# Kernel optimization log

Hardware: AMD Instinct MI355X
Metric: run time of the kernel (lower is better)

Reference implementation:

```python
import jax, jax.numpy as jnp
import numpy as np

SQRT3 = float(np.sqrt(3.0))
TWO_PI = float(2.0 * np.pi)


def _safe_sqrt(x):
    return jnp.sqrt(jnp.clip(x, 1e-5))


def _matern(Q):
    # Matern 3/2 on the (already halved) quadratic form, matching torch matern()
    t = SQRT3 * _safe_sqrt(Q)
    return (1.0 + t) * jnp.exp(-t)


def _pairwise_kernel(x1, kp1, x2, kp2, scale):
    """Fused prob_product_quad + prob_product_constant + matern.

    x: [B,N,2] coords; kp: [B,N,3] = (e00, e11, e01) of SPD 2x2 E per point.
    Returns K [B,N,M].
    """
    a1, b1, c1 = kp1[..., 0], kp1[..., 1], kp1[..., 2]  # e00, e11, e01
    a2, b2, c2 = kp2[..., 0], kp2[..., 1], kp2[..., 2]
    det1 = a1 * b1 - c1 * c1  # det2x2(E1) [B,N]
    det2 = a2 * b2 - c2 * c2  # [B,M]
    s00 = a1[:, :, None] + a2[:, None, :]  # E1_00 + E2_00  [B,N,M]
    s11 = b1[:, :, None] + b2[:, None, :]
    s01 = c1[:, :, None] + c2[:, None, :]
    sdet = s00 * s11 - s01 * s01  # det(E1+E2)
    d = x1[:, :, None, :] - x2[:, None, :, :]  # [B,N,M,2]
    d0, d1 = d[..., 0], d[..., 1]
    Q = (s11 * d0 * d0 - 2.0 * s01 * d0 * d1 + s00 * d1 * d1) / sdet * 0.5
    C = 2.0 * (det1 ** 0.25)[:, :, None] * (det2 ** 0.25)[:, None, :] / _safe_sqrt(sdet)
    return _matern(Q) * C * scale


def _diag_kernel(kp, scale):
    # diagonal_prob_product: Q = 0, C = 2*sqrt(det E)/safe_sqrt(det(2E))
    a, b, c = kp[..., 0], kp[..., 1], kp[..., 2]
    det = a * b - c * c
    det2E = 4.0 * det  # det(2E) for 2x2
    C = 2.0 * jnp.sqrt(det) / _safe_sqrt(det2E)
    Q = jnp.zeros_like(C)
    return C * _matern(Q) * scale  # [B,N]


def setup_inputs() -> dict:
    key = jax.random.key(0)
    ks = jax.random.split(key, 8)
    B, N, M = 2, 1024, 16384

    def kparams(k, n):
        u = jax.random.uniform(k, (B, n, 3), dtype=jnp.float32)
        a = 0.5 + u[..., 0]
        b = 0.5 + u[..., 1]
        c = 0.2 * (u[..., 2] - 0.5)  # |c| small -> SPD
        return jnp.stack([a, b, c], axis=-1)

    coords_train = jax.random.uniform(ks[0], (B, N, 2), dtype=jnp.float32) * 512.0 / 64.0
    coords_test = jax.random.uniform(ks[1], (B, M, 2), dtype=jnp.float32) * 512.0 / 64.0
    kernel_params_train = kparams(ks[2], N)
    kernel_params_test = kparams(ks[3], M)
    y_train = jax.random.uniform(ks[4], (B, N, 1), dtype=jnp.float32) * 10.0
    var = 0.01 + 0.1 * jax.random.uniform(ks[5], (B, N), dtype=jnp.float32)
    mean = jnp.zeros((B, 1, 1), dtype=jnp.float32)
    scale_param = jnp.zeros((1,), dtype=jnp.float32)
    return {
        "coords_train": coords_train,
        "kernel_params_train": kernel_params_train,
        "coords_test": coords_test,
        "kernel_params_test": kernel_params_test,
        "y_train": y_train,
        "var": var,
        "mean": mean,
        "scale_param": scale_param,
    }


def reference(coords_train, kernel_params_train, coords_test, kernel_params_test,
              y_train, var, mean, scale_param):
    scale_prior = 1.0
    scale = scale_prior * jnp.exp(scale_param[0])  # CovarianceModule.get_scale
    B, N = coords_train.shape[0], coords_train.shape[1]

    # CovarianceModule / CrossCovarianceModule / DiagonalCovarianceModule
    K_nn = _pairwise_kernel(coords_train, kernel_params_train,
                            coords_train, kernel_params_train, scale)  # [B,N,N]
    K_nm = _pairwise_kernel(coords_train, kernel_params_train,
                            coords_test, kernel_params_test, scale)    # [B,N,M]
    K_mm_diag = _diag_kernel(kernel_params_test, scale)                 # [B,M]

    # GpSparseModule: A = K_nn + diag(var); chol; alpha = A^{-1}(y-mean); NLML
    eye = jnp.eye(N, dtype=K_nn.dtype)
    A = K_nn + var[..., None] * eye
    L = jnp.linalg.cholesky(A)
    y_centered = y_train - mean
    alpha = jax.scipy.linalg.cho_solve((L, True), y_centered)  # [B,N,1]
    data_fit = jnp.sum(y_centered * alpha, axis=1)             # [B,1]
    data_term = 0.5 * jnp.sum(data_fit, axis=1)                # [B]
    complexity_term = jnp.sum(jnp.log(jnp.diagonal(L, axis1=-2, axis2=-1)), axis=1)
    constant_term = 0.5 * N * np.log(TWO_PI)
    nlml = data_term + complexity_term + constant_term

    # GpDenseModule: predictive mean/variance at test points
    pred_mean = mean + jnp.einsum('bnm,bnk->bmk', K_nm, alpha)  # [B,M,1]
    v = jax.scipy.linalg.cho_solve((L, True), K_nm)             # [B,N,M]
    pred_var = (K_mm_diag - jnp.sum(K_nm * v, axis=1))[..., None]  # [B,M,1]
    return pred_mean, pred_var, nlml
```

## Files before the change

### kernel.cpp

```cpp
#include <hip/hip_runtime.h>
#include <math.h>

namespace {
constexpr int kB = 2;
constexpr int kN = 1024;
constexpr int kM = 16384;
constexpr float kSqrt3 = 1.7320508075688772f;

constexpr size_t A_BYTES = (size_t)kB * kN * kN * 4;
constexpr size_t DG_BYTES = (size_t)kB * 8 * 128 * 128 * 4;
constexpr size_t Z_BYTES = (size_t)kB * kN * 4;
constexpr size_t LH_BYTES = (size_t)kB * kN * kN * 2;
constexpr size_t DH_BYTES = (size_t)kB * 8 * 128 * 128 * 2;
constexpr size_t A_OFF = 0;
constexpr size_t DG_OFF = A_OFF + A_BYTES;
constexpr size_t Z_OFF = DG_OFF + DG_BYTES;
constexpr size_t LH_OFF = Z_OFF + Z_BYTES;
constexpr size_t LL_OFF = LH_OFF + LH_BYTES;
constexpr size_t DH_OFF = LL_OFF + LH_BYTES;
constexpr size_t DL_OFF = DH_OFF + DH_BYTES;
constexpr size_t WS_BYTES = DL_OFF + DH_BYTES;
}

typedef __attribute__((ext_vector_type(8))) short short8v;
typedef __attribute__((ext_vector_type(4))) float floatx4;

__device__ __forceinline__ float b16f(unsigned short h) {
  return __uint_as_float(((unsigned)h) << 16);
}
__device__ __forceinline__ unsigned short b16rn(float x) {
  unsigned u = __float_as_uint(x);
  unsigned r = u + 0x7FFFu + ((u >> 16) & 1u);
  return (unsigned short)(r >> 16);
}
__device__ __forceinline__ void split_bf16(float x, unsigned short& h, unsigned short& l) {
  unsigned u = __float_as_uint(x);
  h = (unsigned short)(u >> 16);
  float rem = x - b16f(h);
  l = (unsigned short)(__float_as_uint(rem) >> 16);
}
__device__ __forceinline__ void pack2(float v0, float v1, unsigned& hw, unsigned& lw) {
  unsigned u0 = __float_as_uint(v0), u1 = __float_as_uint(v1);
  unsigned h0 = u0 & 0xFFFF0000u;
  unsigned h1 = u1 & 0xFFFF0000u;
  hw = (h0 >> 16) | h1;
  float r0 = v0 - __uint_as_float(h0);
  float r1 = v1 - __uint_as_float(h1);
  lw = (__float_as_uint(r0) >> 16) | (__float_as_uint(r1) & 0xFFFF0000u);
}

__device__ __forceinline__ float pair_kernel(
    float x0, float x1, float a1, float b1, float c1,
    float y0, float y1, float a2, float b2, float c2, float scale) {
  float det1 = a1 * b1 - c1 * c1;
  float det2 = a2 * b2 - c2 * c2;
  float s00 = a1 + a2, s11 = b1 + b2, s01 = c1 + c2;
  float sdet = s00 * s11 - s01 * s01;
  float d0 = x0 - y0, d1 = x1 - y1;
  float quad = s11 * d0 * d0 - 2.0f * s01 * d0 * d1 + s00 * d1 * d1;
  float Q = __fdividef(0.5f * quad, sdet);
  float x3 = 3.0f * fmaxf(Q, 1e-5f);
  float t = x3 * rsqrtf(x3);
  float C = 2.0f * sqrtf(sqrtf(det1)) * sqrtf(sqrtf(det2)) * rsqrtf(fmaxf(sdet, 1e-5f));
  return (1.0f + t) * __expf(-t) * C * scale;
}

__global__ __launch_bounds__(256) void build_A(
    const float* __restrict__ xt, const float* __restrict__ pt,
    const float* __restrict__ var, const float* __restrict__ sp,
    float* __restrict__ A) {
  int idx = blockIdx.x * 256 + threadIdx.x;
  int b = idx / (kN * kN);
  int r = (idx / kN) % kN;
  int c = idx % kN;
  float scale = __expf(sp[0]);
  const float* x1 = xt + ((size_t)b * kN + r) * 2;
  const float* p1 = pt + ((size_t)b * kN + r) * 3;
  const float* x2 = xt + ((size_t)b * kN + c) * 2;
  const float* p2 = pt + ((size_t)b * kN + c) * 3;
  float k = pair_kernel(x1[0], x1[1], p1[0], p1[1], p1[2],
                        x2[0], x2[1], p2[0], p2[1], p2[2], scale);
  if (r == c) k += var[b * kN + r];
  A[(size_t)idx] = k;
}

__device__ __forceinline__ void tri_decode(int idx, int& ti, int& tj) {
  float f = sqrtf(8.0f * (float)idx + 1.0f);
  int t0 = (int)((f - 1.0f) * 0.5f);
  while (t0 * (t0 + 1) / 2 > idx) --t0;
  while ((t0 + 1) * (t0 + 2) / 2 <= idx) ++t0;
  ti = t0;
  tj = idx - t0 * (t0 + 1) / 2;
}

__global__ __launch_bounds__(1024, 1) void chol_panel(float* __restrict__ A,
                                                      float* __restrict__ Dg,
                                                      unsigned short* __restrict__ Dh,
                                                      unsigned short* __restrict__ Dl, int p) {
  __shared__ float At[128 * 132];
  __shared__ float Dt[128 * 132];
  __shared__ float Tt[3 * 32 * 33];
  int b = blockIdx.x, t = threadIdx.x;
  float* Ab = A + (size_t)b * kN * kN;
  int r0 = p * 128;
#pragma unroll
  for (int q = 0; q < 4; ++q) {
    int idx = t + 1024 * q;
    int r = idx >> 5, c4 = idx & 31;
    *(float4*)&At[r * 132 + c4 * 4] = *(const float4*)&Ab[(size_t)(r0 + r) * kN + r0 + c4 * 4];
  }
  __syncthreads();
  int wave = t >> 6, lane = t & 63;
  int row0 = lane, row1 = lane + 64;
  for (int kb = 0; kb < 16; ++kb) {
    int K0 = kb * 8;
    int Kp = K0 - 8;
    if (kb > 0) {
      if (wave == 0) {
        int rr = lane >> 3, cc = lane & 7;
        float s = 0.0f;
#pragma unroll
        for (int e = 0; e < 8; ++e)
          s += At[(K0 + rr) * 132 + Kp + e] * At[(K0 + cc) * 132 + Kp + e];
        At[(K0 + rr) * 132 + K0 + cc] -= s;
      } else {
        int n = 120 - 8 * kb;
        int nt = n >> 2;
        int ntt = nt * (nt + 1) / 2;
        int base = K0 + 8;
        for (int idx = t - 64; idx < ntt; idx += 960) {
          int ti, tj;
          tri_decode(idx, ti, tj);
          int i0 = base + ti * 4, j0 = base + tj * 4;
          float Li[4][8], Lj[4][8];
#pragma unroll
          for (int r = 0; r < 4; ++r) {
            *(float4*)&Li[r][0] = *(const float4*)&At[(i0 + r) * 132 + Kp];
            *(float4*)&Li[r][4] = *(const float4*)&At[(i0 + r) * 132 + Kp + 4];
            *(float4*)&Lj[r][0] = *(const float4*)&At[(j0 + r) * 132 + Kp];
            *(float4*)&Lj[r][4] = *(const float4*)&At[(j0 + r) * 132 + Kp + 4];
          }
#pragma unroll
          for (int r = 0; r < 4; ++r) {
            float4 cv = *(const float4*)&At[(i0 + r) * 132 + j0];
            float cc4[4] = {cv.x, cv.y, cv.z, cv.w};
#pragma unroll
            for (int c = 0; c < 4; ++c) {
              float s = 0.0f;
#pragma unroll
              for (int e = 0; e < 8; ++e) s += Li[r][e] * Lj[c][e];
              cc4[c] -= s;
            }
            float4 ov = {cc4[0], cc4[1], cc4[2], cc4[3]};
            *(float4*)&At[(i0 + r) * 132 + j0] = ov;
          }
        }
      }
    }
    __syncthreads();
    if (wave == 0) {
      float rA0[8], rA1[8];
      *(float4*)&rA0[0] = *(const float4*)&At[row0 * 132 + K0];
      *(float4*)&rA0[4] = *(const float4*)&At[row0 * 132 + K0 + 4];
      *(float4*)&rA1[0] = *(const float4*)&At[row1 * 132 + K0];
      *(float4*)&rA1[4] = *(const float4*)&At[row1 * 132 + K0 + 4];
      if (kb > 0) {
        float pA0[8], pA1[8];
        *(float4*)&pA0[0] = *(const float4*)&At[row0 * 132 + Kp];
        *(float4*)&pA0[4] = *(const float4*)&At[row0 * 132 + Kp + 4];
        *(float4*)&pA1[0] = *(const float4*)&At[row1 * 132 + Kp];
        *(float4*)&pA1[4] = *(const float4*)&At[row1 * 132 + Kp + 4];
#pragma unroll
        for (int j = 0; j < 8; ++j) {
          float s0 = 0.0f, s1 = 0.0f;
#pragma unroll
          for (int e = 0; e < 8; ++e) {
            float pj = At[(K0 + j) * 132 + Kp + e];
            s0 += pA0[e] * pj;
            s1 += pA1[e] * pj;
          }
          rA0[j] -= s0;
          rA1[j] -= s1;
        }
      }
      float L11[8][8], idg[8];
#pragma unroll
      for (int r = 0; r < 8; ++r) {
        *(float4*)&L11[r][0] = *(const float4*)&At[(K0 + r) * 132 + K0];
        *(float4*)&L11[r][4] = *(const float4*)&At[(K0 + r) * 132 + K0 + 4];
      }
#pragma unroll
      for (int c = 0; c < 8; ++c) {
        float d = sqrtf(L11[c][c]);
        float iv = 1.0f / d;
        idg[c] = iv;
        L11[c][c] = d;
#pragma unroll
        for (int i = c + 1; i < 8; ++i) L11[i][c] *= iv;
#pragma unroll
        for (int j = c + 1; j < 8; ++j)
#pragma unroll
          for (int i = j; i < 8; ++i) L11[i][j] -= L11[i][c] * L11[j][c];
      }
      if (row0 >= K0 + 8) {
#pragma unroll
        for (int c = 0; c < 8; ++c) {
          float s = rA0[c];
#pragma unroll
          for (int j = 0; j < c; ++j) s -= rA0[j] * L11[c][j];
          rA0[c] = s * idg[c];
        }
      } else if (row0 >= K0) {
#pragma unroll
        for (int rr = 0; rr < 8; ++rr)
          if (row0 - K0 == rr) {
#pragma unroll
            for (int e = 0; e < 8; ++e) rA0[e] = (e <= rr) ? L11[rr][e] : 0.0f;
          }
      }
      if (row1 >= K0 + 8) {
#pragma unroll
        for (int c = 0; c < 8; ++c) {
          float s = rA1[c];
#pragma unroll
          for (int j = 0; j < c; ++j) s -= rA1[j] * L11[c][j];
          rA1[c] = s * idg[c];
        }
      } else if (row1 >= K0) {
#pragma unroll
        for (int rr = 0; rr < 8; ++rr)
          if (row1 - K0 == rr) {
#pragma unroll
            for (int e = 0; e < 8; ++e) rA1[e] = (e <= rr) ? L11[rr][e] : 0.0f;
          }
      }
      if (row0 >= K0) {
        float4 v0 = {rA0[0], rA0[1], rA0[2], rA0[3]};
        float4 v1 = {rA0[4], rA0[5], rA0[6], rA0[7]};
        *(float4*)&At[row0 * 132 + K0] = v0;
        *(float4*)&At[row0 * 132 + K0 + 4] = v1;
      }
      if (row1 >= K0) {
        float4 v0 = {rA1[0], rA1[1], rA1[2], rA1[3]};
        float4 v1 = {rA1[4], rA1[5], rA1[6], rA1[7]};
        *(float4*)&At[row1 * 132 + K0] = v0;
        *(float4*)&At[row1 * 132 + K0 + 4] = v1;
      }
    }
    __syncthreads();
  }
  if (t < 128) {
    int q = t >> 5, c = t & 31, bse = q * 32;
    float x[32];
#pragma unroll
    for (int r = 0; r < 32; ++r) {
      float s = (r == c) ? 1.0f : 0.0f;
#pragma unroll
      for (int j = 0; j < 32; ++j)
        if (j < r) s -= At[(bse + r) * 132 + bse + j] * x[j];
      x[r] = (r < c) ? 0.0f : s / At[(bse + r) * 132 + bse + r];
    }
#pragma unroll
    for (int r = 0; r < 32; ++r) Dt[(bse + r) * 132 + bse + c] = x[r];
  }
  __syncthreads();
  {
    int r = t >> 5, cl = t & 31;
    for (int s = 1; s <= 3; ++s) {
      for (int blk = 0; blk < 4 - s; ++blk) {
        int J = blk, I = J + s;
        float sum = 0.0f;
        for (int K = J; K < I; ++K)
          for (int j = 0; j < 32; ++j)
            sum += At[(I * 32 + r) * 132 + K * 32 + j] * Dt[(K * 32 + j) * 132 + J * 32 + cl];
        Tt[blk * (32 * 33) + r * 33 + cl] = sum;
      }
      __syncthreads();
      for (int blk = 0; blk < 4 - s; ++blk) {
        int J = blk, I = J + s;
        float sum = 0.0f;
        for (int j = 0; j < 32; ++j)
          sum += Dt[(I * 32 + r) * 132 + I * 32 + j] * Tt[blk * (32 * 33) + j * 33 + cl];
        Dt[(I * 32 + r) * 132 + J * 32 + cl] = -sum;
      }
      __syncthreads();
    }
  }
#pragma unroll
  for (int q = 0; q < 4; ++q) {
    int jj = t + 1024 * q;
    int r = jj >> 5, ch = jj & 31;
    int c0 = ch * 4;
    float4 v = *(const float4*)&At[r * 132 + c0];
    v.x = (c0 + 0 <= r) ? v.x : 0.0f;
    v.y = (c0 + 1 <= r) ? v.y : 0.0f;
    v.z = (c0 + 2 <= r) ? v.z : 0.0f;
    v.w = (c0 + 3 <= r) ? v.w : 0.0f;
    *(float4*)&Ab[(size_t)(r0 + r) * kN + r0 + c0] = v;
  }
  float* Db = Dg + (size_t)(b * 8 + p) * 16384;
  unsigned short* Dhb = Dh + (size_t)(b * 8 + p) * 16384;
  unsigned short* Dlb = Dl + (size_t)(b * 8 + p) * 16384;
#pragma unroll
  for (int q = 0; q < 4; ++q) {
    int jj = t + 1024 * q;
    int r = jj >> 5, ch = jj & 31;
    int c0 = ch * 4;
    float4 v = *(const float4*)&Dt[r * 132 + c0];
    v.x = (c0 + 0 <= r) ? v.x : 0.0f;
    v.y = (c0 + 1 <= r) ? v.y : 0.0f;
    v.z = (c0 + 2 <= r) ? v.z : 0.0f;
    v.w = (c0 + 3 <= r) ? v.w : 0.0f;
    *(float4*)&Db[r * 128 + c0] = v;
    float vv[4] = {v.x, v.y, v.z, v.w};
    unsigned short hs[4], ls[4];
#pragma unroll
    for (int e = 0; e < 4; ++e) split_bf16(vv[e], hs[e], ls[e]);
    *(ushort4*)&Dhb[r * 128 + c0] = make_ushort4(hs[0], hs[1], hs[2], hs[3]);
    *(ushort4*)&Dlb[r * 128 + c0] = make_ushort4(ls[0], ls[1], ls[2], ls[3]);
  }
}

__global__ __launch_bounds__(256) void chol_trsm(float* __restrict__ A,
                                                 const float* __restrict__ Dg,
                                                 unsigned short* __restrict__ Lh, int p) {
  __shared__ float At[128 * 129];
  __shared__ float Dt[128 * 129];
  int b = blockIdx.y, rb = blockIdx.x;
  int rs = (p + 1 + rb) * 128;
  float* Ab = A + (size_t)b * kN * kN;
  const float* Db = Dg + (size_t)(b * 8 + p) * 16384;
  int t = threadIdx.x;
  for (int q = 0; q < 64; ++q) {
    int li = t + 256 * q;
    int r = li >> 7, cc = li & 127;
    At[r * 129 + cc] = Ab[(size_t)(rs + r) * kN + p * 128 + cc];
    Dt[r * 129 + cc] = Db[r * 128 + cc];
  }
  __syncthreads();
  int tx = t & 15, ty = t >> 4;
  float acc[8][8] = {};
  for (int j = 0; j < 128; ++j) {
    float a[8], d[8];
#pragma unroll
    for (int q = 0; q < 8; ++q) a[q] = At[(ty * 8 + q) * 129 + j];
#pragma unroll
    for (int q = 0; q < 8; ++q) d[q] = Dt[(tx * 8 + q) * 129 + j];
#pragma unroll
    for (int qr = 0; qr < 8; ++qr)
#pragma unroll
      for (int qc = 0; qc < 8; ++qc) acc[qr][qc] = fmaf(a[qr], d[qc], acc[qr][qc]);
  }
#pragma unroll
  for (int qr = 0; qr < 8; ++qr)
#pragma unroll
    for (int qc = 0; qc < 8; ++qc) {
      float v = acc[qr][qc];
      Ab[(size_t)(rs + ty * 8 + qr) * kN + p * 128 + tx * 8 + qc] = v;
      size_t lo = ((size_t)b * kN + rs + ty * 8 + qr) * kN + p * 128 + tx * 8 + qc;
      Lh[lo] = b16rn(-v);
    }
}

__global__ __launch_bounds__(256) void chol_syrk(float* __restrict__ A, int p) {
  __shared__ float L1t[128 * 129];
  __shared__ float L2t[128 * 129];
  int b = blockIdx.y;
  int pid = blockIdx.x;
  int bi = 0;
  while ((bi + 1) * (bi + 2) / 2 <= pid) ++bi;
  int bj = pid - bi * (bi + 1) / 2;
  int rs1 = (p + 1 + bi) * 128, rs2 = (p + 1 + bj) * 128;
  float* Ab = A + (size_t)b * kN * kN;
  int t = threadIdx.x;
  for (int q = 0; q < 64; ++q) {
    int li = t + 256 * q;
    int r = li >> 7, cc = li & 127;
    L1t[r * 129 + cc] = Ab[(size_t)(rs1 + r) * kN + p * 128 + cc];
    L2t[r * 129 + cc] = Ab[(size_t)(rs2 + r) * kN + p * 128 + cc];
  }
  __syncthreads();
  int tx = t & 15, ty = t >> 4;
  float acc[8][8] = {};
  for (int j = 0; j < 128; ++j) {
    float a[8], d[8];
#pragma unroll
    for (int q = 0; q < 8; ++q) a[q] = L1t[(ty * 8 + q) * 129 + j];
#pragma unroll
    for (int q = 0; q < 8; ++q) d[q] = L2t[(tx * 8 + q) * 129 + j];
#pragma unroll
    for (int qr = 0; qr < 8; ++qr)
#pragma unroll
      for (int qc = 0; qc < 8; ++qc) acc[qr][qc] = fmaf(a[qr], d[qc], acc[qr][qc]);
  }
#pragma unroll
  for (int qr = 0; qr < 8; ++qr)
#pragma unroll
    for (int qc = 0; qc < 8; ++qc) {
      size_t o = (size_t)(rs1 + ty * 8 + qr) * kN + rs2 + tx * 8 + qc;
      Ab[o] -= acc[qr][qc];
    }
}

__global__ __launch_bounds__(1024) void solve_small(
    const float* __restrict__ A, const float* __restrict__ Dg,
    const float* __restrict__ y, const float* __restrict__ meanp,
    float* __restrict__ zbuf, float* __restrict__ out) {
  __shared__ float Ls[128 * 132];
  __shared__ __align__(16) float zs[1024];
  __shared__ float ts[128];
  __shared__ float part[128 * 9];
  __shared__ float red[1024];
  int b = blockIdx.x, t = threadIdx.x;
  int row = t & 127, g = t >> 7;
  const float* Ab = A + (size_t)b * kN * kN;
  float mv = meanp[b];
  zs[t] = y[b * kN + t] - mv;
  __syncthreads();
  for (int i = 0; i < 8; ++i) {
    float ps = 0.0f;
    for (int k = 0; k < i; ++k) {
#pragma unroll
      for (int q = 0; q < 4; ++q) {
        int li = t + 1024 * q;
        int r = li >> 5, c4 = li & 31;
        *(float4*)&Ls[r * 132 + c4 * 4] =
            *(const float4*)&Ab[(size_t)(i * 128 + r) * kN + k * 128 + c4 * 4];
      }
      __syncthreads();
      const float* Lr = &Ls[row * 132 + g * 16];
      const float* zk = &zs[k * 128 + g * 16];
#pragma unroll
      for (int c = 0; c < 16; c += 4) {
        float4 lv = *(const float4*)&Lr[c];
        float4 zv = *(const float4*)&zk[c];
        ps += lv.x * zv.x + lv.y * zv.y + lv.z * zv.z + lv.w * zv.w;
      }
      __syncthreads();
    }
    part[row * 9 + g] = ps;
    {
      const float* Db = Dg + (size_t)(b * 8 + i) * 16384;
#pragma unroll
      for (int q = 0; q < 4; ++q) {
        int li = t + 1024 * q;
        int r = li >> 5, c4 = li & 31;
        *(float4*)&Ls[r * 132 + c4 * 4] = *(const float4*)&Db[r * 128 + c4 * 4];
      }
    }
    __syncthreads();
    if (g == 0) {
      float acc = zs[i * 128 + row];
#pragma unroll
      for (int gg = 0; gg < 8; ++gg) acc -= part[row * 9 + gg];
      ts[row] = acc;
    }
    __syncthreads();
    float s = 0.0f;
    int c0 = g * 16, c1 = min(c0 + 16, row + 1);
    for (int c = c0; c < c1; ++c) s += Ls[row * 132 + c] * ts[c];
    part[row * 9 + g] = s;
    __syncthreads();
    if (g == 0) {
      float zv = 0.0f;
#pragma unroll
      for (int gg = 0; gg < 8; ++gg) zv += part[row * 9 + gg];
      zs[i * 128 + row] = zv;
    }
    __syncthreads();
  }
  red[t] = zs[t] * zs[t];
  __syncthreads();
  for (int s = 512; s > 0; s >>= 1) {
    if (t < s) red[t] += red[t + s];
    __syncthreads();
  }
  float dfs = red[0];
  __syncthreads();
  red[t] = logf(Ab[(size_t)t * kN + t]);
  __syncthreads();
  for (int s = 512; s > 0; s >>= 1) {
    if (t < s) red[t] += red[t + s];
    __syncthreads();
  }
  if (t == 0)
    out[2 * kB * kM + b] = 0.5f * dfs + red[0] + 0.5f * 1024.0f * logf(6.283185307179586f);
  zbuf[b * kN + t] = zs[t];
}

__global__ __launch_bounds__(256, 2) void fused_mfma(
    const unsigned short* __restrict__ Lh,
    const unsigned short* __restrict__ Dh, const unsigned short* __restrict__ Dl,
    const float* __restrict__ xt, const float* __restrict__ pt,
    const float* __restrict__ xs, const float* __restrict__ ps,
    const float* __restrict__ sp, const float* __restrict__ meanp,
    const float* __restrict__ zbuf, float* __restrict__ out) {
  __shared__ unsigned short Th[32 * 144];
  __shared__ unsigned short Tl[32 * 144];
  __shared__ float trp[128 * 6];
  __shared__ float tp[32 * 6];
  __shared__ float zs[128];
  __shared__ float red[32 * 16 * 2];
  int bid = blockIdx.x;
  int xcd = bid & 7;
  int b = xcd >> 2;
  int mt = (xcd & 3) * 128 + (bid >> 3);
  int t = threadIdx.x;
  int lane = t & 63, wave = t >> 6;
  int lrow = lane & 15, kgrp = lane >> 4;
  float scale = __expf(sp[0]);
  if (t < 32) {
    int mg = mt * 32 + t;
    float x0 = xs[((size_t)b * kM + mg) * 2 + 0];
    float x1 = xs[((size_t)b * kM + mg) * 2 + 1];
    float a = ps[((size_t)b * kM + mg) * 3 + 0];
    float bb = ps[((size_t)b * kM + mg) * 3 + 1];
    float c = ps[((size_t)b * kM + mg) * 3 + 2];
    float det2 = a * bb - c * c;
    tp[t * 6 + 0] = x0; tp[t * 6 + 1] = x1; tp[t * 6 + 2] = a;
    tp[t * 6 + 3] = bb; tp[t * 6 + 4] = c; tp[t * 6 + 5] = sqrtf(sqrtf(det2));
  }
  floatx4 W[8][2][2];
#pragma unroll
  for (int i = 0; i < 8; ++i)
#pragma unroll
    for (int rf = 0; rf < 2; ++rf)
#pragma unroll
      for (int cf = 0; cf < 2; ++cf) W[i][rf][cf] = (floatx4){0.f, 0.f, 0.f, 0.f};
  float pma[2] = {0.f, 0.f}, s2a[2] = {0.f, 0.f};

#define FUSED_K_STEP(KC)                                                                   \
  {                                                                                        \
    constexpr int k = (KC);                                                                \
    __syncthreads();                                                                       \
    if (t < 128) {                                                                         \
      size_t n = (size_t)b * kN + k * 128 + t;                                             \
      float x0 = xt[n * 2 + 0];                                                            \
      float x1 = xt[n * 2 + 1];                                                            \
      float a = pt[n * 3 + 0];                                                             \
      float bb = pt[n * 3 + 1];                                                            \
      float c = pt[n * 3 + 2];                                                             \
      float det1 = a * bb - c * c;                                                         \
      trp[t * 6 + 0] = x0; trp[t * 6 + 1] = x1; trp[t * 6 + 2] = a;                        \
      trp[t * 6 + 3] = bb; trp[t * 6 + 4] = c;                                             \
      trp[t * 6 + 5] = 2.0f * scale * sqrtf(sqrtf(det1));                                  \
      zs[t] = zbuf[n];                                                                     \
    }                                                                                      \
    __syncthreads();                                                                       \
    _Pragma("unroll")                                                                      \
    for (int rf = 0; rf < 2; ++rf) {                                                       \
      int n0 = wave * 32 + rf * 16 + kgrp * 4;                                             \
      float nx0[4], nx1[4], na[4], nb[4], nc[4], nc1[4];                                   \
      _Pragma("unroll")                                                                    \
      for (int r = 0; r < 4; ++r) {                                                        \
        int n = n0 + r;                                                                    \
        nx0[r] = trp[n * 6 + 0]; nx1[r] = trp[n * 6 + 1]; na[r] = trp[n * 6 + 2];          \
        nb[r] = trp[n * 6 + 3]; nc[r] = trp[n * 6 + 4]; nc1[r] = trp[n * 6 + 5];           \
      }                                                                                    \
      _Pragma("unroll")                                                                    \
      for (int cf = 0; cf < 2; ++cf) {                                                     \
        int m = cf * 16 + lrow;                                                            \
        float mx0 = tp[m * 6 + 0], mx1 = tp[m * 6 + 1], ma = tp[m * 6 + 2];                \
        float mb = tp[m * 6 + 3], mc = tp[m * 6 + 4], mq = tp[m * 6 + 5];                  \
        float Tv[4];                                                                       \
        _Pragma("unroll")                                                                  \
        for (int r = 0; r < 4; ++r) {                                                      \
          float s00 = na[r] + ma, s11 = nb[r] + mb, s01 = nc[r] + mc;                      \
          float sdet = s00 * s11 - s01 * s01;                                              \
          float d0 = nx0[r] - mx0, d1 = nx1[r] - mx1;                                      \
          float quad = s11 * d0 * d0 - 2.0f * s01 * d0 * d1 + s00 * d1 * d1;               \
          float Q = __fdividef(0.5f * quad, sdet);                                         \
          float x3 = 3.0f * fmaxf(Q, 1e-5f);                                               \
          float tt = x3 * rsqrtf(x3);                                                      \
          float Kv = (1.0f + tt) * __expf(-tt) * nc1[r] * (mq * rsqrtf(fmaxf(sdet, 1e-5f))); \
          Tv[r] = Kv + W[k][rf][cf][r];                                                    \
        }                                                                                  \
        unsigned hw[2], lw[2];                                                             \
        pack2(Tv[0], Tv[1], hw[0], lw[0]);                                                 \
        pack2(Tv[2], Tv[3], hw[1], lw[1]);                                                 \
        int off = m * 144 + n0;                                                            \
        *(uint2*)&Th[off] = make_uint2(hw[0], hw[1]);                                      \
        *(uint2*)&Tl[off] = make_uint2(lw[0], lw[1]);                                      \
      }                                                                                    \
    }                                                                                      \
    __syncthreads();                                                                       \
    floatx4 wk[2][2];                                                                      \
    _Pragma("unroll")                                                                      \
    for (int rf = 0; rf < 2; ++rf)                                                         \
      _Pragma("unroll")                                                                    \
      for (int cf = 0; cf < 2; ++cf) wk[rf][cf] = (floatx4){0.f, 0.f, 0.f, 0.f};           \
    {                                                                                      \
      const unsigned short* Dhb = Dh + (size_t)(b * 8 + k) * 16384;                        \
      const unsigned short* Dlb = Dl + (size_t)(b * 8 + k) * 16384;                        \
      _Pragma("unroll")                                                                    \
      for (int ks = 0; ks < 4; ++ks) {                                                     \
        short8v bh[2], bl[2];                                                              \
        _Pragma("unroll")                                                                  \
        for (int cf = 0; cf < 2; ++cf) {                                                   \
          int boff = (cf * 16 + lrow) * 144 + ks * 32 + kgrp * 8;                          \
          bh[cf] = *(const short8v*)&Th[boff];                                             \
          bl[cf] = *(const short8v*)&Tl[boff];                                             \
        }                                                                                  \
        short8v ah[2], al[2];                                                              \
        _Pragma("unroll")                                                                  \
        for (int rf = 0; rf < 2; ++rf) {                                                   \
          size_t aoff = (size_t)(wave * 32 + rf * 16 + lrow) * 128 + ks * 32 + kgrp * 8;   \
          ah[rf] = *(const short8v*)&Dhb[aoff];                                            \
          al[rf] = *(const short8v*)&Dlb[aoff];                                            \
        }                                                                                  \
        _Pragma("unroll")                                                                  \
        for (int rf = 0; rf < 2; ++rf)                                                     \
          _Pragma("unroll")                                                                \
          for (int cf = 0; cf < 2; ++cf) {                                                 \
            wk[rf][cf] = __builtin_amdgcn_mfma_f32_16x16x32_bf16(ah[rf], bh[cf], wk[rf][cf], 0, 0, 0); \
            wk[rf][cf] = __builtin_amdgcn_mfma_f32_16x16x32_bf16(ah[rf], bl[cf], wk[rf][cf], 0, 0, 0); \
            wk[rf][cf] = __builtin_amdgcn_mfma_f32_16x16x32_bf16(al[rf], bh[cf], wk[rf][cf], 0, 0, 0); \
          }                                                                                \
      }                                                                                    \
    }                                                                                      \
    __syncthreads();                                                                       \
    _Pragma("unroll")                                                                      \
    for (int rf = 0; rf < 2; ++rf) {                                                       \
      int n0 = wave * 32 + rf * 16 + kgrp * 4;                                             \
      _Pragma("unroll")                                                                    \
      for (int cf = 0; cf < 2; ++cf) {                                                     \
        int m = cf * 16 + lrow;                                                            \
        float wv[4];                                                                       \
        _Pragma("unroll")                                                                  \
        for (int r = 0; r < 4; ++r) {                                                      \
          wv[r] = wk[rf][cf][r];                                                           \
          pma[cf] = fmaf(wv[r], zs[n0 + r], pma[cf]);                                      \
          s2a[cf] = fmaf(wv[r], wv[r], s2a[cf]);                                           \
        }                                                                                  \
        unsigned hw[2], lw[2];                                                             \
        pack2(wv[0], wv[1], hw[0], lw[0]);                                                 \
        pack2(wv[2], wv[3], hw[1], lw[1]);                                                 \
        int off = m * 144 + n0;                                                            \
        *(uint2*)&Th[off] = make_uint2(hw[0], hw[1]);                                      \
        *(uint2*)&Tl[off] = make_uint2(lw[0], lw[1]);                                      \
      }                                                                                    \
    }                                                                                      \
    __syncthreads();                                                                       \
    __builtin_amdgcn_s_setprio(1);                                                         \
    _Pragma("unroll")                                                                      \
    for (int ks = 0; ks < 4; ++ks) {                                                       \
      short8v bh[2], bl[2];                                                                \
      _Pragma("unroll")                                                                    \
      for (int cf = 0; cf < 2; ++cf) {                                                     \
        int boff = (cf * 16 + lrow) * 144 + ks * 32 + kgrp * 8;                            \
        bh[cf] = *(const short8v*)&Th[boff];                                               \
        bl[cf] = *(const short8v*)&Tl[boff];                                               \
      }                                                                                    \
      _Pragma("unroll")                                                                    \
      for (int i = k + 1; i < 8; ++i) {                                                    \
        short8v ah[2];                                                                     \
        _Pragma("unroll")                                                                  \
        for (int rf = 0; rf < 2; ++rf) {                                                   \
          size_t ro = (size_t)b * kN + i * 128 + wave * 32 + rf * 16 + lrow;               \
          size_t aoff = ro * kN + k * 128 + ks * 32 + kgrp * 8;                            \
          ah[rf] = *(const short8v*)&Lh[aoff];                                             \
        }                                                                                  \
        _Pragma("unroll")                                                                  \
        for (int rf = 0; rf < 2; ++rf)                                                     \
          _Pragma("unroll")                                                                \
          for (int cf = 0; cf < 2; ++cf) {                                                 \
            W[i][rf][cf] = __builtin_amdgcn_mfma_f32_16x16x32_bf16(ah[rf], bh[cf], W[i][rf][cf], 0, 0, 0); \
            W[i][rf][cf] = __builtin_amdgcn_mfma_f32_16x16x32_bf16(ah[rf], bl[cf], W[i][rf][cf], 0, 0, 0); \
          }                                                                                \
      }                                                                                    \
    }                                                                                      \
    __builtin_amdgcn_s_setprio(0);                                                         \
  }

  FUSED_K_STEP(0)
  FUSED_K_STEP(1)
  FUSED_K_STEP(2)
  FUSED_K_STEP(3)
  FUSED_K_STEP(4)
  FUSED_K_STEP(5)
  FUSED_K_STEP(6)
  FUSED_K_STEP(7)
#undef FUSED_K_STEP

  __syncthreads();
#pragma unroll
  for (int cf = 0; cf < 2; ++cf) {
    int m = cf * 16 + lrow;
    red[m * 16 + wave * 4 + kgrp] = pma[cf];
    red[512 + m * 16 + wave * 4 + kgrp] = s2a[cf];
  }
  __syncthreads();
  if (t < 32) {
    float pm = 0.f, s2 = 0.f;
#pragma unroll
    for (int j = 0; j < 16; ++j) {
      pm += red[t * 16 + j];
      s2 += red[512 + t * 16 + j];
    }
    int mg = mt * 32 + t;
    float a = tp[t * 6 + 2], bb = tp[t * 6 + 3], c = tp[t * 6 + 4];
    float det = a * bb - c * c;
    float C = 2.0f * sqrtf(det) * rsqrtf(fmaxf(4.0f * det, 1e-5f));
    float t0 = kSqrt3 * sqrtf(1e-5f);
    float mat = (1.0f + t0) * __expf(-t0);
    float kd = C * mat * scale;
    out[b * kM + mg] = meanp[b] + pm;
    out[kB * kM + b * kM + mg] = kd - s2;
  }
}

extern "C" void kernel_launch(void* const* d_in, const int* in_sizes, int n_in,
                              void* d_out, int out_size, void* d_ws, size_t ws_size,
                              hipStream_t stream) {
  const float* xt = (const float*)d_in[0];
  const float* pt = (const float*)d_in[1];
  const float* xs = (const float*)d_in[2];
  const float* ps = (const float*)d_in[3];
  const float* y = (const float*)d_in[4];
  const float* var = (const float*)d_in[5];
  const float* meanp = (const float*)d_in[6];
  const float* sp = (const float*)d_in[7];
  float* out = (float*)d_out;
  char* ws = (char*)d_ws;
  if (ws_size < WS_BYTES) return;

  float* A = (float*)(ws + A_OFF);
  float* Dg = (float*)(ws + DG_OFF);
  float* zbuf = (float*)(ws + Z_OFF);
  unsigned short* Lh = (unsigned short*)(ws + LH_OFF);
  unsigned short* Dh = (unsigned short*)(ws + DH_OFF);
  unsigned short* Dl = (unsigned short*)(ws + DL_OFF);

  build_A<<<(kB * kN * kN) / 256, 256, 0, stream>>>(xt, pt, var, sp, A);
  for (int p = 0; p < 8; ++p) {
    chol_panel<<<kB, 1024, 0, stream>>>(A, Dg, Dh, Dl, p);
    if (p < 7) {
      int nt = 7 - p;
      chol_trsm<<<dim3(nt, kB), 256, 0, stream>>>(A, Dg, Lh, p);
      chol_syrk<<<dim3(nt * (nt + 1) / 2, kB), 256, 0, stream>>>(A, p);
    }
  }
  solve_small<<<kB, 1024, 0, stream>>>(A, Dg, y, meanp, zbuf, out);
  fused_mfma<<<kB * 512, 256, 0, stream>>>(Lh, Dh, Dl, xt, pt, xs, ps,
                                           sp, meanp, zbuf, out);
}
```

Before: 1.138 ms.

## Fuse next diagonal panel factorization into SYRK block and shrink panel to 256 threads

Result: slower. 1.355 ms (+19.1%).

```diff
diff --git a/kernel.cpp b/kernel.cpp
--- a/kernel.cpp
+++ b/kernel.cpp
@@ -20,6 +20,13 @@
 constexpr size_t DH_OFF = LL_OFF + LH_BYTES;
 constexpr size_t DL_OFF = DH_OFF + DH_BYTES;
 constexpr size_t WS_BYTES = DL_OFF + DH_BYTES;
+
+constexpr int PAN_AT = 0;
+constexpr int PAN_DT = 16896;
+constexpr int PAN_TT = 33792;
+constexpr int PAN_FLOATS = 36960;
+constexpr int SYR_L1 = 0;
+constexpr int SYR_L2 = 16512;
 }
 
 typedef __attribute__((ext_vector_type(8))) short short8v;
@@ -93,21 +100,20 @@
   tj = idx - t0 * (t0 + 1) / 2;
 }
 
-__global__ __launch_bounds__(1024, 1) void chol_panel(float* __restrict__ A,
-                                                      float* __restrict__ Dg,
-                                                      unsigned short* __restrict__ Dh,
-                                                      unsigned short* __restrict__ Dl, int p) {
-  __shared__ float At[128 * 132];
-  __shared__ float Dt[128 * 132];
-  __shared__ float Tt[3 * 32 * 33];
-  int b = blockIdx.x, t = threadIdx.x;
-  float* Ab = A + (size_t)b * kN * kN;
-  int r0 = p * 128;
-#pragma unroll
-  for (int q = 0; q < 4; ++q) {
-    int idx = t + 1024 * q;
-    int r = idx >> 5, c4 = idx & 31;
-    *(float4*)&At[r * 132 + c4 * 4] = *(const float4*)&Ab[(size_t)(r0 + r) * kN + r0 + c4 * 4];
+__device__ void panel_factor_256(float* __restrict__ sh, float* __restrict__ Ab,
+                                 float* __restrict__ Db, unsigned short* __restrict__ Dhb,
+                                 unsigned short* __restrict__ Dlb, int r0, int t,
+                                 bool preStaged) {
+  float* At = sh + PAN_AT;
+  float* Dt = sh + PAN_DT;
+  float* Tt = sh + PAN_TT;
+  if (!preStaged) {
+#pragma unroll
+    for (int q = 0; q < 16; ++q) {
+      int idx = t + 256 * q;
+      int r = idx >> 5, c4 = idx & 31;
+      *(float4*)&At[r * 132 + c4 * 4] = *(const float4*)&Ab[(size_t)(r0 + r) * kN + r0 + c4 * 4];
+    }
   }
   __syncthreads();
   int wave = t >> 6, lane = t & 63;
@@ -128,7 +134,7 @@
         int nt = n >> 2;
         int ntt = nt * (nt + 1) / 2;
         int base = K0 + 8;
-        for (int idx = t - 64; idx < ntt; idx += 960) {
+        for (int idx = t - 64; idx < ntt; idx += 192) {
           int ti, tj;
           tri_decode(idx, ti, tj);
           int i0 = base + ti * 4, j0 = base + tj * 4;
@@ -265,30 +271,36 @@
   }
   __syncthreads();
   {
-    int r = t >> 5, cl = t & 31;
+    int rb_ = t >> 5, cl = t & 31;
     for (int s = 1; s <= 3; ++s) {
       for (int blk = 0; blk < 4 - s; ++blk) {
         int J = blk, I = J + s;
-        float sum = 0.0f;
-        for (int K = J; K < I; ++K)
-          for (int j = 0; j < 32; ++j)
-            sum += At[(I * 32 + r) * 132 + K * 32 + j] * Dt[(K * 32 + j) * 132 + J * 32 + cl];
-        Tt[blk * (32 * 33) + r * 33 + cl] = sum;
+        for (int rr = 0; rr < 4; ++rr) {
+          int r = rr * 8 + rb_;
+          float sum = 0.0f;
+          for (int K = J; K < I; ++K)
+            for (int j = 0; j < 32; ++j)
+              sum += At[(I * 32 + r) * 132 + K * 32 + j] * Dt[(K * 32 + j) * 132 + J * 32 + cl];
+          Tt[blk * (32 * 33) + r * 33 + cl] = sum;
+        }
       }
       __syncthreads();
       for (int blk = 0; blk < 4 - s; ++blk) {
         int J = blk, I = J + s;
-        float sum = 0.0f;
-        for (int j = 0; j < 32; ++j)
-          sum += Dt[(I * 32 + r) * 132 + I * 32 + j] * Tt[blk * (32 * 33) + j * 33 + cl];
-        Dt[(I * 32 + r) * 132 + J * 32 + cl] = -sum;
+        for (int rr = 0; rr < 4; ++rr) {
+          int r = rr * 8 + rb_;
+          float sum = 0.0f;
+          for (int j = 0; j < 32; ++j)
+            sum += Dt[(I * 32 + r) * 132 + I * 32 + j] * Tt[blk * (32 * 33) + j * 33 + cl];
+          Dt[(I * 32 + r) * 132 + J * 32 + cl] = -sum;
+        }
       }
       __syncthreads();
     }
   }
 #pragma unroll
-  for (int q = 0; q < 4; ++q) {
-    int jj = t + 1024 * q;
+  for (int q = 0; q < 16; ++q) {
+    int jj = t + 256 * q;
     int r = jj >> 5, ch = jj & 31;
     int c0 = ch * 4;
     float4 v = *(const float4*)&At[r * 132 + c0];
@@ -298,12 +310,9 @@
     v.w = (c0 + 3 <= r) ? v.w : 0.0f;
     *(float4*)&Ab[(size_t)(r0 + r) * kN + r0 + c0] = v;
   }
-  float* Db = Dg + (size_t)(b * 8 + p) * 16384;
-  unsigned short* Dhb = Dh + (size_t)(b * 8 + p) * 16384;
-  unsigned short* Dlb = Dl + (size_t)(b * 8 + p) * 16384;
-#pragma unroll
-  for (int q = 0; q < 4; ++q) {
-    int jj = t + 1024 * q;
+#pragma unroll
+  for (int q = 0; q < 16; ++q) {
+    int jj = t + 256 * q;
     int r = jj >> 5, ch = jj & 31;
     int c0 = ch * 4;
     float4 v = *(const float4*)&Dt[r * 132 + c0];
@@ -319,6 +328,17 @@
     *(ushort4*)&Dhb[r * 128 + c0] = make_ushort4(hs[0], hs[1], hs[2], hs[3]);
     *(ushort4*)&Dlb[r * 128 + c0] = make_ushort4(ls[0], ls[1], ls[2], ls[3]);
   }
+}
+
+__global__ __launch_bounds__(256, 1) void chol_panel0(float* __restrict__ A,
+                                                      float* __restrict__ Dg,
+                                                      unsigned short* __restrict__ Dh,
+                                                      unsigned short* __restrict__ Dl, int p) {
+  extern __shared__ float sh[];
+  int b = blockIdx.x, t = threadIdx.x;
+  panel_factor_256(sh, A + (size_t)b * kN * kN, Dg + (size_t)(b * 8 + p) * 16384,
+                   Dh + (size_t)(b * 8 + p) * 16384, Dl + (size_t)(b * 8 + p) * 16384,
+                   p * 128, t, false);
 }
 
 __global__ __launch_bounds__(256) void chol_trsm(float* __restrict__ A,
@@ -362,9 +382,14 @@
     }
 }
 
-__global__ __launch_bounds__(256) void chol_syrk(float* __restrict__ A, int p) {
-  __shared__ float L1t[128 * 129];
-  __shared__ float L2t[128 * 129];
+__global__ __launch_bounds__(256, 1) void chol_syrk_panel(float* __restrict__ A,
+                                                          float* __restrict__ Dg,
+                                                          unsigned short* __restrict__ Dh,
+                                                          unsigned short* __restrict__ Dl,
+                                                          int p) {
+  extern __shared__ float sh[];
+  float* L1t = sh + SYR_L1;
+  float* L2t = sh + SYR_L2;
   int b = blockIdx.y;
   int pid = blockIdx.x;
   int bi = 0;
@@ -393,13 +418,29 @@
 #pragma unroll
       for (int qc = 0; qc < 8; ++qc) acc[qr][qc] = fmaf(a[qr], d[qc], acc[qr][qc]);
   }
+  if (pid != 0) {
+#pragma unroll
+    for (int qr = 0; qr < 8; ++qr)
+#pragma unroll
+      for (int qc = 0; qc < 8; ++qc) {
+        size_t o = (size_t)(rs1 + ty * 8 + qr) * kN + rs2 + tx * 8 + qc;
+        Ab[o] -= acc[qr][qc];
+      }
+    return;
+  }
+  __syncthreads();
+  float* At = sh + PAN_AT;
 #pragma unroll
   for (int qr = 0; qr < 8; ++qr)
 #pragma unroll
     for (int qc = 0; qc < 8; ++qc) {
-      size_t o = (size_t)(rs1 + ty * 8 + qr) * kN + rs2 + tx * 8 + qc;
-      Ab[o] -= acc[qr][qc];
-    }
+      float ao = Ab[(size_t)(rs1 + ty * 8 + qr) * kN + rs2 + tx * 8 + qc];
+      At[(ty * 8 + qr) * 132 + tx * 8 + qc] = ao - acc[qr][qc];
+    }
+  int pn = p + 1;
+  panel_factor_256(sh, Ab, Dg + (size_t)(b * 8 + pn) * 16384,
+                   Dh + (size_t)(b * 8 + pn) * 16384, Dl + (size_t)(b * 8 + pn) * 16384,
+                   pn * 128, t, true);
 }
 
 __global__ __launch_bounds__(1024) void solve_small(
@@ -495,8 +536,8 @@
     const float* __restrict__ xs, const float* __restrict__ ps,
     const float* __restrict__ sp, const float* __restrict__ meanp,
     const float* __restrict__ zbuf, float* __restrict__ out) {
-  __shared__ unsigned short Th[32 * 144];
-  __shared__ unsigned short Tl[32 * 144];
+  __shared__ unsigned short Th[32 * 136];
+  __shared__ unsigned short Tl[32 * 136];
   __shared__ float trp[128 * 6];
   __shared__ float tp[32 * 6];
   __shared__ float zs[128];
@@ -578,7 +619,7 @@
         unsigned hw[2], lw[2];                                                             \
         pack2(Tv[0], Tv[1], hw[0], lw[0]);                                                 \
         pack2(Tv[2], Tv[3], hw[1], lw[1]);                                                 \
-        int off = m * 144 + n0;                                                            \
+        int off = m * 136 + n0;                                                            \
         *(uint2*)&Th[off] = make_uint2(hw[0], hw[1]);                                      \
         *(uint2*)&Tl[off] = make_uint2(lw[0], lw[1]);                                      \
       }                                                                                    \
@@ -597,7 +638,7 @@
         short8v bh[2], bl[2];                                                              \
         _Pragma("unroll")                                                                  \
         for (int cf = 0; cf < 2; ++cf) {                                                   \
-          int boff = (cf * 16 + lrow) * 144 + ks * 32 + kgrp * 8;                          \
+          int boff = (cf * 16 + lrow) * 136 + ks * 32 + kgrp * 8;                          \
           bh[cf] = *(const short8v*)&Th[boff];                                             \
           bl[cf] = *(const short8v*)&Tl[boff];                                             \
         }                                                                                  \
@@ -635,7 +676,7 @@
         unsigned hw[2], lw[2];                                                             \
         pack2(wv[0], wv[1], hw[0], lw[0]);                                                 \
         pack2(wv[2], wv[3], hw[1], lw[1]);                                                 \
-        int off = m * 144 + n0;                                                            \
+        int off = m * 136 + n0;                                                            \
         *(uint2*)&Th[off] = make_uint2(hw[0], hw[1]);                                      \
         *(uint2*)&Tl[off] = make_uint2(lw[0], lw[1]);                                      \
       }                                                                                    \
@@ -647,7 +688,7 @@
       short8v bh[2], bl[2];                                                                \
       _Pragma("unroll")                                                                    \
       for (int cf = 0; cf < 2; ++cf) {                                                     \
-        int boff = (cf * 16 + lrow) * 144 + ks * 32 + kgrp * 8;                            \
+        int boff = (cf * 16 + lrow) * 136 + ks * 32 + kgrp * 8;                            \
         bh[cf] = *(const short8v*)&Th[boff];                                               \
         bl[cf] = *(const short8v*)&Tl[boff];                                               \
       }                                                                                    \
@@ -731,14 +772,15 @@
   unsigned short* Dh = (unsigned short*)(ws + DH_OFF);
   unsigned short* Dl = (unsigned short*)(ws + DL_OFF);
 
+  const size_t panLds = PAN_FLOATS * sizeof(float);
+
   build_A<<<(kB * kN * kN) / 256, 256, 0, stream>>>(xt, pt, var, sp, A);
-  for (int p = 0; p < 8; ++p) {
-    chol_panel<<<kB, 1024, 0, stream>>>(A, Dg, Dh, Dl, p);
-    if (p < 7) {
-      int nt = 7 - p;
-      chol_trsm<<<dim3(nt, kB), 256, 0, stream>>>(A, Dg, Lh, p);
-      chol_syrk<<<dim3(nt * (nt + 1) / 2, kB), 256, 0, stream>>>(A, p);
-    }
+  chol_panel0<<<kB, 256, panLds, stream>>>(A, Dg, Dh, Dl, 0);
+  for (int p = 0; p < 7; ++p) {
+    int nt = 7 - p;
+    chol_trsm<<<dim3(nt, kB), 256, 0, stream>>>(A, Dg, Lh, p);
+    int npairs = nt * (nt + 1) / 2;
+    chol_syrk_panel<<<dim3(npairs, kB), 256, panLds, stream>>>(A, Dg, Dh, Dl, p);
   }
   solve_small<<<kB, 1024, 0, stream>>>(A, Dg, y, meanp, zbuf, out);
   fused_mfma<<<kB * 512, 256, 0, stream>>>(Lh, Dh, Dl, xt, pt, xs, ps,
```

## Double-buffer train-point parameters, shrink LDS pad, simplify Matern math

Applied to the files above, without the earlier changes.

New measurement: 1.135 ms (median of 3 runs). Within noise of the previous version (-0.3%).

```diff
diff --git a/kernel.cpp b/kernel.cpp
--- a/kernel.cpp
+++ b/kernel.cpp
@@ -56,12 +56,12 @@
   float det2 = a2 * b2 - c2 * c2;
   float s00 = a1 + a2, s11 = b1 + b2, s01 = c1 + c2;
   float sdet = s00 * s11 - s01 * s01;
+  float rsq = rsqrtf(fmaxf(sdet, 1e-5f));
   float d0 = x0 - y0, d1 = x1 - y1;
   float quad = s11 * d0 * d0 - 2.0f * s01 * d0 * d1 + s00 * d1 * d1;
-  float Q = __fdividef(0.5f * quad, sdet);
-  float x3 = 3.0f * fmaxf(Q, 1e-5f);
-  float t = x3 * rsqrtf(x3);
-  float C = 2.0f * sqrtf(sqrtf(det1)) * sqrtf(sqrtf(det2)) * rsqrtf(fmaxf(sdet, 1e-5f));
+  float u = 1.5f * quad * rsq * rsq;
+  float t = sqrtf(fmaxf(u, 3e-5f));
+  float C = 2.0f * sqrtf(sqrtf(det1)) * sqrtf(sqrtf(det2)) * rsq;
   return (1.0f + t) * __expf(-t) * C * scale;
 }
 
@@ -495,11 +495,11 @@
     const float* __restrict__ xs, const float* __restrict__ ps,
     const float* __restrict__ sp, const float* __restrict__ meanp,
     const float* __restrict__ zbuf, float* __restrict__ out) {
-  __shared__ unsigned short Th[32 * 144];
-  __shared__ unsigned short Tl[32 * 144];
-  __shared__ float trp[128 * 6];
+  __shared__ unsigned short Th[32 * 136];
+  __shared__ unsigned short Tl[32 * 136];
+  __shared__ float trp2[2][128 * 6];
+  __shared__ float zs2[2][128];
   __shared__ float tp[32 * 6];
-  __shared__ float zs[128];
   __shared__ float red[32 * 16 * 2];
   int bid = blockIdx.x;
   int xcd = bid & 7;
@@ -520,6 +520,19 @@
     tp[t * 6 + 0] = x0; tp[t * 6 + 1] = x1; tp[t * 6 + 2] = a;
     tp[t * 6 + 3] = bb; tp[t * 6 + 4] = c; tp[t * 6 + 5] = sqrtf(sqrtf(det2));
   }
+  if (t < 128) {
+    size_t n = (size_t)b * kN + t;
+    float x0 = xt[n * 2 + 0];
+    float x1 = xt[n * 2 + 1];
+    float a = pt[n * 3 + 0];
+    float bb = pt[n * 3 + 1];
+    float c = pt[n * 3 + 2];
+    float det1 = a * bb - c * c;
+    trp2[0][t * 6 + 0] = x0; trp2[0][t * 6 + 1] = x1; trp2[0][t * 6 + 2] = a;
+    trp2[0][t * 6 + 3] = bb; trp2[0][t * 6 + 4] = c;
+    trp2[0][t * 6 + 5] = 2.0f * scale * sqrtf(sqrtf(det1));
+    zs2[0][t] = zbuf[n];
+  }
   floatx4 W[8][2][2];
 #pragma unroll
   for (int i = 0; i < 8; ++i)
@@ -528,25 +541,13 @@
 #pragma unroll
       for (int cf = 0; cf < 2; ++cf) W[i][rf][cf] = (floatx4){0.f, 0.f, 0.f, 0.f};
   float pma[2] = {0.f, 0.f}, s2a[2] = {0.f, 0.f};
+  __syncthreads();
 
 #define FUSED_K_STEP(KC)                                                                   \
   {                                                                                        \
     constexpr int k = (KC);                                                                \
-    __syncthreads();                                                                       \
-    if (t < 128) {                                                                         \
-      size_t n = (size_t)b * kN + k * 128 + t;                                             \
-      float x0 = xt[n * 2 + 0];                                                            \
-      float x1 = xt[n * 2 + 1];                                                            \
-      float a = pt[n * 3 + 0];                                                             \
-      float bb = pt[n * 3 + 1];                                                            \
-      float c = pt[n * 3 + 2];                                                             \
-      float det1 = a * bb - c * c;                                                         \
-      trp[t * 6 + 0] = x0; trp[t * 6 + 1] = x1; trp[t * 6 + 2] = a;                        \
-      trp[t * 6 + 3] = bb; trp[t * 6 + 4] = c;                                             \
-      trp[t * 6 + 5] = 2.0f * scale * sqrtf(sqrtf(det1));                                  \
-      zs[t] = zbuf[n];                                                                     \
-    }                                                                                      \
-    __syncthreads();                                                                       \
+    const float* trp = trp2[k & 1];                                                        \
+                                                           \
     _Pragma("unroll")                                                                      \
     for (int rf = 0; rf < 2; ++rf) {                                                       \
       int n0 = wave * 32 + rf * 16 + kgrp * 4;                                             \
@@ -567,23 +568,38 @@
         for (int r = 0; r < 4; ++r) {                                                      \
           float s00 = na[r] + ma, s11 = nb[r] + mb, s01 = nc[r] + mc;                      \
           float sdet = s00 * s11 - s01 * s01;                                              \
+          float rsq = rsqrtf(fmaxf(sdet, 1e-5f));                                          \
           float d0 = nx0[r] - mx0, d1 = nx1[r] - mx1;                                      \
           float quad = s11 * d0 * d0 - 2.0f * s01 * d0 * d1 + s00 * d1 * d1;               \
-          float Q = __fdividef(0.5f * quad, sdet);                                         \
-          float x3 = 3.0f * fmaxf(Q, 1e-5f);                                               \
-          float tt = x3 * rsqrtf(x3);                                                      \
-          float Kv = (1.0f + tt) * __expf(-tt) * nc1[r] * (mq * rsqrtf(fmaxf(sdet, 1e-5f))); \
+          float u = 1.5f * quad * rsq * rsq;                                               \
+          float tt = sqrtf(fmaxf(u, 3e-5f));                                               \
+          float Kv = (1.0f + tt) * __expf(-tt) * nc1[r] * (mq * rsq);                      \
           Tv[r] = Kv + W[k][rf][cf][r];                                                    \
         }                                                                                  \
         unsigned hw[2], lw[2];                                                             \
         pack2(Tv[0], Tv[1], hw[0], lw[0]);                                                 \
         pack2(Tv[2], Tv[3], hw[1], lw[1]);                                                 \
-        int off = m * 144 + n0;                                                            \
+        int off = m * 136 + n0;                                                            \
         *(uint2*)&Th[off] = make_uint2(hw[0], hw[1]);                                      \
         *(uint2*)&Tl[off] = make_uint2(lw[0], lw[1]);                                      \
       }                                                                                    \
     }                                                                                      \
-    __syncthreads();                                                                       \
+    __syncthreads();                                                                \
+                                 \
+    if (k < 7 && t < 128) {                                                                \
+      size_t n = (size_t)b * kN + (k + 1) * 128 + t;                                       \
+      float x0 = xt[n * 2 + 0];                                                            \
+      float x1 = xt[n * 2 + 1];                                                            \
+      float a = pt[n * 3 + 0];                                                             \
+      float bb = pt[n * 3 + 1];                                                            \
+      float c = pt[n * 3 + 2];                                                             \
+      float det1 = a * bb - c * c;                                                         \
+      trp2[(k + 1) & 1][t * 6 + 0] = x0; trp2[(k + 1) & 1][t * 6 + 1] = x1;                \
+      trp2[(k + 1) & 1][t * 6 + 2] = a;  trp2[(k + 1) & 1][t * 6 + 3] = bb;                \
+      trp2[(k + 1) & 1][t * 6 + 4] = c;                                                    \
+      trp2[(k + 1) & 1][t * 6 + 5] = 2.0f * scale * sqrtf(sqrtf(det1));                    \
+      zs2[(k + 1) & 1][t] = zbuf[n];                                                       \
+    }                                                                                      \
     floatx4 wk[2][2];                                                                      \
     _Pragma("unroll")                                                                      \
     for (int rf = 0; rf < 2; ++rf)                                                         \
@@ -597,7 +613,7 @@
         short8v bh[2], bl[2];                                                              \
         _Pragma("unroll")                                                                  \
         for (int cf = 0; cf < 2; ++cf) {                                                   \
-          int boff = (cf * 16 + lrow) * 144 + ks * 32 + kgrp * 8;                          \
+          int boff = (cf * 16 + lrow) * 136 + ks * 32 + kgrp * 8;                          \
           bh[cf] = *(const short8v*)&Th[boff];                                             \
           bl[cf] = *(const short8v*)&Tl[boff];                                             \
         }                                                                                  \
@@ -618,7 +634,8 @@
           }                                                                                \
       }                                                                                    \
     }                                                                                      \
-    __syncthreads();                                                                       \
+    __syncthreads();                                                                \
+                                               \
     _Pragma("unroll")                                                                      \
     for (int rf = 0; rf < 2; ++rf) {                                                       \
       int n0 = wave * 32 + rf * 16 + kgrp * 4;                                             \
@@ -629,25 +646,26 @@
         _Pragma("unroll")                                                                  \
         for (int r = 0; r < 4; ++r) {                                                      \
           wv[r] = wk[rf][cf][r];                                                           \
-          pma[cf] = fmaf(wv[r], zs[n0 + r], pma[cf]);                                      \
+          pma[cf] = fmaf(wv[r], zs2[k & 1][n0 + r], pma[cf]);                              \
           s2a[cf] = fmaf(wv[r], wv[r], s2a[cf]);                                           \
         }                                                                                  \
         unsigned hw[2], lw[2];                                                             \
         pack2(wv[0], wv[1], hw[0], lw[0]);                                                 \
         pack2(wv[2], wv[3], hw[1], lw[1]);                                                 \
-        int off = m * 144 + n0;                                                            \
+        int off = m * 136 + n0;                                                            \
         *(uint2*)&Th[off] = make_uint2(hw[0], hw[1]);                                      \
         *(uint2*)&Tl[off] = make_uint2(lw[0], lw[1]);                                      \
       }                                                                                    \
     }                                                                                      \
-    __syncthreads();                                                                       \
+    __syncthreads();                                                                \
+                                                            \
     __builtin_amdgcn_s_setprio(1);                                                         \
     _Pragma("unroll")                                                                      \
     for (int ks = 0; ks < 4; ++ks) {                                                       \
       short8v bh[2], bl[2];                                                                \
       _Pragma("unroll")                                                                    \
       for (int cf = 0; cf < 2; ++cf) {                                                     \
-        int boff = (cf * 16 + lrow) * 144 + ks * 32 + kgrp * 8;                            \
+        int boff = (cf * 16 + lrow) * 136 + ks * 32 + kgrp * 8;                            \
         bh[cf] = *(const short8v*)&Th[boff];                                               \
         bl[cf] = *(const short8v*)&Tl[boff];                                               \
       }                                                                                    \
@@ -670,6 +688,7 @@
       }                                                                                    \
     }                                                                                      \
     __builtin_amdgcn_s_setprio(0);                                                         \
+    __syncthreads();             \
   }
 
   FUSED_K_STEP(0)
@@ -682,7 +701,6 @@
   FUSED_K_STEP(7)
 #undef FUSED_K_STEP
 
-  __syncthreads();
 #pragma unroll
   for (int cf = 0; cf < 2; ++cf) {
     int m = cf * 16 + lrow;
```
